# Kernel optimization log

Measured on AMD Instinct MI355X. Metric: run time of the kernel, lower is better.

The kernel has to match this reference:

```python
import jax, jax.numpy as jnp
import numpy as np


def setup_inputs() -> dict:
    key = jax.random.key(0)
    ks = jax.random.split(key, 9)
    bs, d, K, h = 2048, 128, 256, 256
    s = 0.02  # weight init scale
    return {
        "xhat": jax.random.normal(ks[0], (bs, d), jnp.float32),
        "x": jax.random.normal(ks[1], (bs, d), jnp.float32),
        "codebook": jax.random.normal(ks[2], (K, d), jnp.float32),
        "Wc": jax.random.normal(ks[3], (d, 2 * d), jnp.float32) * s,
        "bc": jnp.zeros((d,), jnp.float32),
        "W1_0": jax.random.normal(ks[4], (h, d), jnp.float32) * s,
        "W2_0": jax.random.normal(ks[5], (d, h), jnp.float32) * s,
        "W1_1": jax.random.normal(ks[6], (h, d), jnp.float32) * s,
        "W2_1": jax.random.normal(ks[7], (d, h), jnp.float32) * s,
    }


def reference(xhat, x, codebook, Wc, bc, W1_0, W2_0, W1_1, W2_1):
    # QINCoStep.encode: evaluate all K codebook candidates per batch element.
    d = xhat.shape[1]
    # MLPconcat on concat([zqs, xhat], -1): split Wc [d, 2d] into codebook and xhat parts,
    # so we never materialize the (bs*K, 2d) concatenated tensor.
    Wz, Wx = Wc[:, :d], Wc[:, d:]
    z = (codebook + codebook @ Wz.T)[None, :, :] + (xhat @ Wx.T)[:, None, :] + bc  # [bs, K, d]
    for W1, W2 in ((W1_0, W2_0), (W1_1, W2_1)):
        z = z + jax.nn.relu(jnp.einsum("bkd,hd->bkh", z, W1)) @ W2.T
    cand = z + xhat[:, None, :]  # [bs, K, d] candidate reconstructions
    dist = jnp.sum(jnp.square(cand - x[:, None, :]), axis=-1)  # [bs, K]
    codes = jnp.argmin(dist, axis=1)  # [bs]
    xhat_next = jnp.take_along_axis(cand, codes[:, None, None], axis=1)[:, 0]  # [bs, d]
    return codes, xhat_next - xhat
```

## Files before the change

kernel.cpp:

```cpp
#include <hip/hip_runtime.h>


typedef short bf8_t __attribute__((ext_vector_type(8)));
typedef float f32x16 __attribute__((ext_vector_type(16)));

__device__ inline unsigned short f2bh(float x) {
    unsigned u = __float_as_uint(x);
    u += 0x7fffu + ((u >> 16) & 1u);
    return (unsigned short)(u >> 16);
}
__device__ inline f32x16 mfma_bf(uint4 a, uint4 b, f32x16 c) {
    bf8_t av = __builtin_bit_cast(bf8_t, a);
    bf8_t bv = __builtin_bit_cast(bf8_t, b);
    return __builtin_amdgcn_mfma_f32_32x32x16_bf16(av, bv, c, 0, 0, 0);
}
__device__ inline unsigned packhi(float x, float y) {
    return __builtin_amdgcn_perm(__float_as_uint(y), __float_as_uint(x), 0x07060302u);
}

#define DELTA 6.0f

__global__ __launch_bounds__(256) void k_prep1(
    const float* __restrict__ Wc,
    const float* __restrict__ W1a, const float* __restrict__ W2a,
    const float* __restrict__ W1b, const float* __restrict__ W2b,
    float* __restrict__ WzT, float* __restrict__ WxT,
    float* __restrict__ W1Ta, float* __restrict__ W2Ta,
    float* __restrict__ W1Tb, float* __restrict__ W2Tb,
    uint4* __restrict__ F)
{
    int g = blockIdx.x * 256 + threadIdx.x;
    if (g < 16384) {
        int j = g >> 7, d = g & 127;
        WzT[g] = Wc[d * 256 + j];
    } else if (g < 32768) {
        int e = g - 16384; int j = e >> 7, d = e & 127;
        WxT[e] = Wc[d * 256 + 128 + j];
    } else if (g < 65536) {
        int e = g - 32768; int d = e >> 8, h = e & 255;
        W1Ta[e] = W1a[h * 128 + d];
    } else if (g < 98304) {
        int e = g - 65536; int h = e >> 7, i = e & 127;
        W2Ta[e] = W2a[i * 256 + h];
    } else if (g < 131072) {
        int e = g - 98304; int d = e >> 8, h = e & 255;
        W1Tb[e] = W1b[h * 128 + d];
    } else if (g < 163840) {
        int e = g - 131072; int h = e >> 7, i = e & 127;
        W2Tb[e] = W2b[i * 256 + h];
    } else if (g < 176128) {
        int idx = g - 163840;
        int mat = idx >> 12, fp = idx & 4095;
        int tile = fp >> 6, lane = fp & 63;
        const float* src;
        if (mat == 1) {
            int mt = tile >> 3, kt = tile & 7;
            src = W1b + (32 * mt + (lane & 31)) * 128 + 16 * kt + 8 * (lane >> 5);
        } else {
            const float* W = (mat == 0) ? W2a : W2b;
            int mt = tile >> 4, kt = tile & 15;
            src = W + (32 * mt + (lane & 31)) * 256 + 16 * kt + 8 * (lane >> 5);
        }
        unsigned short hs[8];
#pragma unroll
        for (int j = 0; j < 8; ++j) hs[j] = f2bh(src[j]);
        uint4 hv;
        hv.x = (unsigned)hs[0] | ((unsigned)hs[1] << 16);
        hv.y = (unsigned)hs[2] | ((unsigned)hs[3] << 16);
        hv.z = (unsigned)hs[4] | ((unsigned)hs[5] << 16);
        hv.w = (unsigned)hs[6] | ((unsigned)hs[7] << 16);
        F[idx] = hv;
    }
}

__global__ __launch_bounds__(256) void k_prep_k(
    const float* __restrict__ cb, const float* __restrict__ bc,
    const float* __restrict__ WzT, const float* __restrict__ W1T0,
    float* __restrict__ z0, float* __restrict__ H1f32)
{
    __shared__ float clds[4][128];
    __shared__ float zlds[4][128];
    const int t = threadIdx.x;
    const int r0 = blockIdx.x * 4;
#pragma unroll
    for (int e = t; e < 512; e += 256)
        clds[e >> 7][e & 127] = cb[(r0 + (e >> 7)) * 128 + (e & 127)];
    __syncthreads();
    {
        const int d = t & 127, r = t >> 7;
        float a0 = bc[d] + clds[r][d], a1 = bc[d] + clds[r + 2][d];
        for (int j = 0; j < 128; ++j) {
            const float w = WzT[j * 128 + d];
            a0 = fmaf(clds[r][j], w, a0);
            a1 = fmaf(clds[r + 2][j], w, a1);
        }
        z0[(r0 + r) * 128 + d] = a0;
        z0[(r0 + r + 2) * 128 + d] = a1;
        zlds[r][d] = a0; zlds[r + 2][d] = a1;
    }
    __syncthreads();
    {
        float a[4] = {0.f, 0.f, 0.f, 0.f};
        for (int d = 0; d < 128; ++d) {
            const float w = W1T0[d * 256 + t];
#pragma unroll
            for (int r = 0; r < 4; ++r) a[r] = fmaf(zlds[r][d], w, a[r]);
        }
        const int kt = t >> 4, half = (t >> 3) & 1, j = t & 7;
#pragma unroll
        for (int r = 0; r < 4; ++r) {
            int k = r0 + r; int kg = k >> 5, col = k & 31;
            H1f32[(((kg * 16 + kt) * 64) + half * 32 + col) * 8 + j] = a[r];
        }
    }
}

__global__ __launch_bounds__(256) void k_prep_b(
    const float* __restrict__ xhat, const float* __restrict__ WxT,
    const float* __restrict__ W1T0,
    float* __restrict__ u, float* __restrict__ U1)
{
    __shared__ float xlds[4][128];
    __shared__ float ulds[4][128];
    const int t = threadIdx.x;
    const int r0 = blockIdx.x * 4;
#pragma unroll
    for (int e = t; e < 512; e += 256)
        xlds[e >> 7][e & 127] = xhat[(r0 + (e >> 7)) * 128 + (e & 127)];
    __syncthreads();
    {
        const int d = t & 127, r = t >> 7;
        float a0 = 0.f, a1 = 0.f;
        for (int j = 0; j < 128; ++j) {
            const float w = WxT[j * 128 + d];
            a0 = fmaf(xlds[r][j], w, a0);
            a1 = fmaf(xlds[r + 2][j], w, a1);
        }
        u[(r0 + r) * 128 + d] = a0;
        u[(r0 + r + 2) * 128 + d] = a1;
        ulds[r][d] = a0; ulds[r + 2][d] = a1;
    }
    __syncthreads();
    {
        float a[4] = {0.f, 0.f, 0.f, 0.f};
        for (int d = 0; d < 128; ++d) {
            const float w = W1T0[d * 256 + t];
#pragma unroll
            for (int r = 0; r < 4; ++r) a[r] = fmaf(ulds[r][d], w, a[r]);
        }
#pragma unroll
        for (int r = 0; r < 4; ++r)
            U1[(r0 + r) * 256 + t] = a[r];
    }
}

__global__ __launch_bounds__(512, 6) void k_dist_approx(
    const float* __restrict__ z0, const float* __restrict__ u,
    const float* __restrict__ xhat, const float* __restrict__ x,
    const float* __restrict__ H1f32, const float* __restrict__ U1,
    const uint4* __restrict__ W2f0, const uint4* __restrict__ W1f1,
    const uint4* __restrict__ W2f1,
    int2* __restrict__ pairs, int* __restrict__ npairs)
{
    __shared__ uint4 Zf[2048];
    __shared__ uint4 Hf[1024];

    const int t = threadIdx.x;
    const int lane = t & 63, wave = t >> 6;
    const int wm = wave & 3, wn = wave >> 2;
    const int l31 = lane & 31, l5 = lane >> 5;
    const int b = blockIdx.x >> 1, q = blockIdx.x & 1;
    const int k0 = q << 7;

    f32x16 zs[2];
    {
        const float* ur = u + b * 128;
#pragma unroll
        for (int g = 0; g < 2; ++g) {
            const int col = ((wn << 1) + g) * 32 + l31;
            const float* zr = z0 + (k0 + col) * 128;
#pragma unroll
            for (int rg = 0; rg < 4; ++rg) {
                const int d0 = 32 * wm + 8 * rg + 4 * l5;
                float4 a = *(const float4*)(zr + d0);
                float4 c = *(const float4*)(ur + d0);
                zs[g][4*rg+0] = a.x + c.x;
                zs[g][4*rg+1] = a.y + c.y;
                zs[g][4*rg+2] = a.z + c.z;
                zs[g][4*rg+3] = a.w + c.w;
            }
        }
    }

#pragma unroll 1
    for (int r = 0; r < 4; ++r) {
        {
            const int kt = 4 * r + wm;
            const float4* up = (const float4*)(U1 + b * 256 + kt * 16 + 8 * l5);
            float4 ua = up[0], ub = up[1];
#pragma unroll
            for (int gi = 0; gi < 2; ++gi) {
                const int cg = (wn << 1) + gi;
                const int kg = (q << 2) + cg;
                const float4* hp = (const float4*)(H1f32 + (((kg * 16 + kt) * 64) + lane) * 8);
                float4 ha = hp[0], hb = hp[1];
                float v0 = fmaxf(ha.x + ua.x, 0.f), v1 = fmaxf(ha.y + ua.y, 0.f);
                float v2 = fmaxf(ha.z + ua.z, 0.f), v3 = fmaxf(ha.w + ua.w, 0.f);
                float v4 = fmaxf(hb.x + ub.x, 0.f), v5 = fmaxf(hb.y + ub.y, 0.f);
                float v6 = fmaxf(hb.z + ub.z, 0.f), v7 = fmaxf(hb.w + ub.w, 0.f);
                uint4 o;
                o.x = packhi(v0, v1); o.y = packhi(v2, v3);
                o.z = packhi(v4, v5); o.w = packhi(v6, v7);
                Hf[((cg << 2) + wm) * 64 + lane] = o;
            }
        }
        __syncthreads();
#pragma unroll
        for (int ktl = 0; ktl < 4; ++ktl) {
            uint4 ah = W2f0[((wm << 4) + 4 * r + ktl) * 64 + lane];
#pragma unroll
            for (int g = 0; g < 2; ++g) {
                uint4 bv = Hf[((((wn << 1) + g) << 2) + ktl) * 64 + lane];
                zs[g] = mfma_bf(ah, bv, zs[g]);
            }
        }
        __syncthreads();
    }

#pragma unroll
    for (int g = 0; g < 2; ++g) {
        const int cg = (wn << 1) + g;
#pragma unroll
        for (int rg = 0; rg < 4; ++rg) {
            uint2 hv;
            hv.x = packhi(zs[g][4*rg+0], zs[g][4*rg+1]);
            hv.y = packhi(zs[g][4*rg+2], zs[g][4*rg+3]);
            uint2* zb2 = (uint2*)&Zf[((cg << 3) + 2 * wm + (rg >> 1)) * 64];
            zb2[(((rg & 1) << 5) + l31) * 2 + l5] = hv;
        }
    }
    __syncthreads();

    const int tile = wave & 1, cg1 = wave >> 1;
#pragma unroll 1
    for (int c = 0; c < 4; ++c) {
        f32x16 acc;
#pragma unroll
        for (int rr = 0; rr < 16; ++rr) acc[rr] = 0.f;
        {
            const uint4* pw1 = W1f1 + ((2 * c + tile) << 3) * 64;
#pragma unroll
            for (int kt = 0; kt < 8; ++kt) {
                uint4 bv = Zf[((cg1 << 3) + kt) * 64 + lane];
                uint4 ah = pw1[kt * 64 + lane];
                acc = mfma_bf(ah, bv, acc);
            }
        }
        __syncthreads();
#pragma unroll
        for (int rg = 0; rg < 4; ++rg) {
            float v0 = fmaxf(acc[4*rg+0], 0.f), v1 = fmaxf(acc[4*rg+1], 0.f);
            float v2 = fmaxf(acc[4*rg+2], 0.f), v3 = fmaxf(acc[4*rg+3], 0.f);
            uint2 hv; hv.x = packhi(v0, v1); hv.y = packhi(v2, v3);
            uint2* hb2 = (uint2*)&Hf[((cg1 << 2) + (tile << 1) + (rg >> 1)) * 64];
            hb2[(((rg & 1) << 5) + l31) * 2 + l5] = hv;
        }
        __syncthreads();
#pragma unroll
        for (int ktl = 0; ktl < 4; ++ktl) {
            uint4 ah = W2f1[((wm << 4) + 4 * c + ktl) * 64 + lane];
#pragma unroll
            for (int g = 0; g < 2; ++g) {
                uint4 bv = Hf[((((wn << 1) + g) << 2) + ktl) * 64 + lane];
                zs[g] = mfma_bf(ah, bv, zs[g]);
            }
        }
    }

    float* red   = (float*)Hf;
    float* sdist = (float*)Hf + 512;
    int*   sk    = (int*)((float*)Hf + 640);
    __syncthreads();
#pragma unroll
    for (int g = 0; g < 2; ++g) {
        float s = 0.f;
        const int col = ((wn << 1) + g) * 32 + l31;
#pragma unroll
        for (int rg = 0; rg < 4; ++rg) {
            const int d0 = 32 * wm + 8 * rg + 4 * l5;
            float4 xh = *(const float4*)(xhat + b * 128 + d0);
            float4 xx = *(const float4*)(x + b * 128 + d0);
            float v;
            v = zs[g][4*rg+0] + xh.x - xx.x; s = fmaf(v, v, s);
            v = zs[g][4*rg+1] + xh.y - xx.y; s = fmaf(v, v, s);
            v = zs[g][4*rg+2] + xh.z - xx.z; s = fmaf(v, v, s);
            v = zs[g][4*rg+3] + xh.w - xx.w; s = fmaf(v, v, s);
        }
        s += __shfl_xor(s, 32, 64);
        if (l5 == 0) red[wm * 128 + col] = s;
    }
    __syncthreads();
    if (t < 128)
        sdist[t] = red[t] + red[128 + t] + red[256 + t] + red[384 + t];
    __syncthreads();
    int base = 0;
    if (wave == 0) {
        float v0 = sdist[lane], v1 = sdist[lane + 64];
        float m = fminf(v0, v1);
#pragma unroll
        for (int off = 32; off > 0; off >>= 1) m = fminf(m, __shfl_xor(m, off, 64));
        const float thr = m + DELTA;
        const unsigned long long below = (1ull << lane) - 1;
        float vv[2] = {v0, v1};
#pragma unroll
        for (int j = 0; j < 2; ++j) {
            bool p = vv[j] <= thr;
            unsigned long long mask = __ballot(p);
            int pos = base + __popcll(mask & below);
            if (p && pos < 8) sk[pos] = k0 + 64 * j + lane;
            base += __popcll(mask);
        }
    }
    __syncthreads();
    if (t == 0) {
        int c = base > 8 ? 8 : base;
        int off = atomicAdd(npairs, c);
        for (int s = 0; s < c; ++s)
            pairs[off + s] = make_int2(b, sk[s]);
    }
}

__global__ __launch_bounds__(256) void k_exact(
    const float* __restrict__ z0, const float* __restrict__ u,
    const float* __restrict__ xhat, const float* __restrict__ x,
    const int2* __restrict__ pairs, const int* __restrict__ npairs,
    const float* __restrict__ W1Ta, const float* __restrict__ W2Ta,
    const float* __restrict__ W1Tb, const float* __restrict__ W2Tb,
    unsigned long long* __restrict__ packed)
{
    __shared__ float z8[8][128];
    __shared__ float h8[8][256];
    __shared__ int pb[8], pk[8];
    __shared__ int scnt;
    __shared__ float part[8][32];
    const int t = threadIdx.x;
    if (t == 0) {
        int np = *npairs; if (np > 32768) np = 32768;
        int c = np - (int)blockIdx.x * 8;
        scnt = c < 0 ? 0 : (c > 8 ? 8 : c);
    }
    __syncthreads();
    const int cnt = scnt;
    if (cnt == 0) return;
    if (t < 8) {
        int idx = blockIdx.x * 8 + (t < cnt ? t : cnt - 1);
        int2 p = pairs[idx];
        pb[t] = p.x; pk[t] = p.y;
    }
    __syncthreads();
#pragma unroll
    for (int n = 0; n < 4; ++n) {
        int e = n * 256 + t; int r = e >> 7, d = e & 127;
        z8[r][d] = z0[pk[r] * 128 + d] + u[pb[r] * 128 + d];
    }
    __syncthreads();
    const float* W1T = W1Ta; const float* W2T = W2Ta;
#pragma unroll 1
    for (int blk = 0; blk < 2; ++blk) {
        float a1[8] = {0.f,0.f,0.f,0.f,0.f,0.f,0.f,0.f};
        for (int d = 0; d < 128; ++d) {
            const float w = W1T[d * 256 + t];
#pragma unroll
            for (int r = 0; r < 8; ++r) a1[r] = fmaf(z8[r][d], w, a1[r]);
        }
#pragma unroll
        for (int r = 0; r < 8; ++r) h8[r][t] = fmaxf(a1[r], 0.f);
        __syncthreads();
        const int ig = t & 127, rg = (t >> 7) * 4;
        float a2[4] = {0.f,0.f,0.f,0.f};
        for (int h = 0; h < 256; ++h) {
            const float w = W2T[h * 128 + ig];
#pragma unroll
            for (int j = 0; j < 4; ++j) a2[j] = fmaf(h8[rg + j][h], w, a2[j]);
        }
        __syncthreads();
#pragma unroll
        for (int j = 0; j < 4; ++j) z8[rg + j][ig] += a2[j];
        __syncthreads();
        W1T = W1Tb; W2T = W2Tb;
    }
    {
        const int r = t >> 5, c = t & 31;
        const int br = pb[r];
        float s = 0.f;
#pragma unroll
        for (int i = 0; i < 4; ++i) {
            int d = c * 4 + i;
            float v = z8[r][d] + xhat[br * 128 + d] - x[br * 128 + d];
            s = fmaf(v, v, s);
        }
        part[r][c] = s;
    }
    __syncthreads();
    if (t < 8 && t < cnt) {
        float s = 0.f;
#pragma unroll
        for (int c2 = 0; c2 < 32; ++c2) s += part[t][c2];
        unsigned long long pk64 = (((unsigned long long)__float_as_uint(s)) << 32)
                                | (unsigned long long)(unsigned)pk[t];
        atomicMin(&packed[pb[t]], pk64);
    }
}

__global__ __launch_bounds__(256) void k_final(
    const float* __restrict__ z0, const float* __restrict__ u,
    const unsigned long long* __restrict__ packed,
    const float* __restrict__ W1Ta, const float* __restrict__ W2Ta,
    const float* __restrict__ W1Tb, const float* __restrict__ W2Tb,
    float* __restrict__ out0, float* __restrict__ outd)
{
    __shared__ float z8[8][128];
    __shared__ float h8[8][256];
    __shared__ int ci[8];
    const int t = threadIdx.x;
    const int b0 = blockIdx.x * 8;
    if (t < 8) {
        int code = (int)(packed[b0 + t] & 0xFFFFFFFFull);
        ci[t] = code;
        out0[b0 + t] = (float)code;
    }
    __syncthreads();
#pragma unroll
    for (int n = 0; n < 4; ++n) {
        int e = n * 256 + t; int r = e >> 7, d = e & 127;
        z8[r][d] = z0[ci[r] * 128 + d] + u[(b0 + r) * 128 + d];
    }
    __syncthreads();
    const float* W1T = W1Ta; const float* W2T = W2Ta;
#pragma unroll 1
    for (int blk = 0; blk < 2; ++blk) {
        float a1[8] = {0.f,0.f,0.f,0.f,0.f,0.f,0.f,0.f};
        for (int d = 0; d < 128; ++d) {
            const float w = W1T[d * 256 + t];
#pragma unroll
            for (int r = 0; r < 8; ++r) a1[r] = fmaf(z8[r][d], w, a1[r]);
        }
#pragma unroll
        for (int r = 0; r < 8; ++r) h8[r][t] = fmaxf(a1[r], 0.f);
        __syncthreads();
        const int ig = t & 127, rg = (t >> 7) * 4;
        float a2[4] = {0.f,0.f,0.f,0.f};
        for (int h = 0; h < 256; ++h) {
            const float w = W2T[h * 128 + ig];
#pragma unroll
            for (int j = 0; j < 4; ++j) a2[j] = fmaf(h8[rg + j][h], w, a2[j]);
        }
        __syncthreads();
#pragma unroll
        for (int j = 0; j < 4; ++j) z8[rg + j][ig] += a2[j];
        __syncthreads();
        W1T = W1Tb; W2T = W2Tb;
    }
#pragma unroll
    for (int n = 0; n < 4; ++n) {
        int e = n * 256 + t; int r = e >> 7, d = e & 127;
        outd[(b0 + r) * 128 + d] = z8[r][d];
    }
}

extern "C" void kernel_launch(void* const* d_in, const int* in_sizes, int n_in,
                              void* d_out, int out_size, void* d_ws, size_t ws_size,
                              hipStream_t stream) {
    const float* xhat = (const float*)d_in[0];
    const float* x    = (const float*)d_in[1];
    const float* cb   = (const float*)d_in[2];
    const float* Wc   = (const float*)d_in[3];
    const float* bc   = (const float*)d_in[4];
    const float* W1_0 = (const float*)d_in[5];
    const float* W2_0 = (const float*)d_in[6];
    const float* W1_1 = (const float*)d_in[7];
    const float* W2_1 = (const float*)d_in[8];
    float* out = (float*)d_out;
    float* ws  = (float*)d_ws;

    float* WzT   = ws + 0;
    float* WxT   = ws + 16384;
    float* W1T0  = ws + 32768;
    float* W2T0  = ws + 65536;
    float* W1T1  = ws + 98304;
    float* W2T1  = ws + 131072;
    float* z0    = ws + 163840;
    float* u     = ws + 196608;
    float* H1f32 = ws + 458752;
    float* U1    = ws + 524288;
    uint4* F     = (uint4*)(ws + 1048576);
    const uint4* W2f0 = F;
    const uint4* W1f1 = F + 4096;
    const uint4* W2f1 = F + 8192;
    int2*  pairs  = (int2*)(ws + 1097728);
    int*   npairs = (int*)(ws + 1163264);
    unsigned long long* packed = (unsigned long long*)(ws + 1163268);

    k_prep1<<<688, 256, 0, stream>>>(Wc, W1_0, W2_0, W1_1, W2_1,
                                     WzT, WxT, W1T0, W2T0, W1T1, W2T1, F);
    k_prep_k<<<64, 256, 0, stream>>>(cb, bc, WzT, W1T0, z0, H1f32);
    k_prep_b<<<512, 256, 0, stream>>>(xhat, WxT, W1T0, u, U1);
    hipMemsetAsync(npairs, 0, 4, stream);
    hipMemsetAsync(packed, 0xFF, 2048 * 8, stream);
    k_dist_approx<<<4096, 512, 0, stream>>>(z0, u, xhat, x, H1f32, U1,
                                            W2f0, W1f1, W2f1, pairs, npairs);
    k_exact<<<4096, 256, 0, stream>>>(z0, u, xhat, x, pairs, npairs,
                                      W1T0, W2T0, W1T1, W2T1, packed);
    k_final<<<256, 256, 0, stream>>>(z0, u, packed,
                                     W1T0, W2T0, W1T1, W2T1, out, out + 2048);
}
```

Baseline: 322.3 us.

## Fuse prep kernels, store bf16 intermediates, merge exact rescoring with final output

Merges the codebook and batch precompute kernels into one launch and stores z0, u, H1 and U1 as bf16 so the approximate-distance kernel reads half the bytes. The atomic pair list, two memsets and the separate exact and final kernels are replaced by per-(batch, half) candidate slots. A single per-batch kernel rescores up to 16 candidates in fp32, picks the argmin and writes the output without 64-bit atomicMin. The DELTA filter margin is widened to offset the extra bf16 rounding, which can admit more candidates and risks borderline argmin decisions.

```diff
diff --git a/kernel.cpp b/kernel.cpp
--- a/kernel.cpp
+++ b/kernel.cpp
@@ -9,6 +9,9 @@
     u += 0x7fffu + ((u >> 16) & 1u);
     return (unsigned short)(u >> 16);
 }
+__device__ inline float bh2f(unsigned short h) {
+    return __uint_as_float(((unsigned)h) << 16);
+}
 __device__ inline f32x16 mfma_bf(uint4 a, uint4 b, f32x16 c) {
     bf8_t av = __builtin_bit_cast(bf8_t, a);
     bf8_t bv = __builtin_bit_cast(bf8_t, b);
@@ -17,8 +20,13 @@
 __device__ inline unsigned packhi(float x, float y) {
     return __builtin_amdgcn_perm(__float_as_uint(y), __float_as_uint(x), 0x07060302u);
 }
-
-#define DELTA 6.0f
+__device__ inline unsigned addrelu2t(unsigned hv, unsigned uv) {
+    float a0 = __uint_as_float(hv << 16) + __uint_as_float(uv << 16);
+    float a1 = __uint_as_float(hv & 0xFFFF0000u) + __uint_as_float(uv & 0xFFFF0000u);
+    return packhi(fmaxf(a0, 0.f), fmaxf(a1, 0.f));
+}
+
+#define DELTA 6.5f
 
 __global__ __launch_bounds__(256) void k_prep1(
     const float* __restrict__ Wc,
@@ -73,30 +81,41 @@
     }
 }
 
-__global__ __launch_bounds__(256) void k_prep_k(
+__global__ __launch_bounds__(256) void k_prep2(
     const float* __restrict__ cb, const float* __restrict__ bc,
-    const float* __restrict__ WzT, const float* __restrict__ W1T0,
-    float* __restrict__ z0, float* __restrict__ H1f32)
+    const float* __restrict__ xhat,
+    const float* __restrict__ WzT, const float* __restrict__ WxT,
+    const float* __restrict__ W1T0,
+    float* __restrict__ z0, unsigned short* __restrict__ z0bf,
+    unsigned short* __restrict__ H1bf,
+    float* __restrict__ u, unsigned short* __restrict__ ubf,
+    unsigned short* __restrict__ U1bf)
 {
-    __shared__ float clds[4][128];
-    __shared__ float zlds[4][128];
+    __shared__ float src[4][128];
+    __shared__ float res[4][128];
     const int t = threadIdx.x;
-    const int r0 = blockIdx.x * 4;
+    const bool krole = blockIdx.x < 64;
+    const int r0 = (krole ? blockIdx.x : (blockIdx.x - 64)) * 4;
+    const float* in = krole ? cb : xhat;
+    const float* WT = krole ? WzT : WxT;
 #pragma unroll
     for (int e = t; e < 512; e += 256)
-        clds[e >> 7][e & 127] = cb[(r0 + (e >> 7)) * 128 + (e & 127)];
+        src[e >> 7][e & 127] = in[(r0 + (e >> 7)) * 128 + (e & 127)];
     __syncthreads();
     {
         const int d = t & 127, r = t >> 7;
-        float a0 = bc[d] + clds[r][d], a1 = bc[d] + clds[r + 2][d];
+        float a0 = krole ? (bc[d] + src[r][d]) : 0.f;
+        float a1 = krole ? (bc[d] + src[r + 2][d]) : 0.f;
         for (int j = 0; j < 128; ++j) {
-            const float w = WzT[j * 128 + d];
-            a0 = fmaf(clds[r][j], w, a0);
-            a1 = fmaf(clds[r + 2][j], w, a1);
-        }
-        z0[(r0 + r) * 128 + d] = a0;
-        z0[(r0 + r + 2) * 128 + d] = a1;
-        zlds[r][d] = a0; zlds[r + 2][d] = a1;
+            const float w = WT[j * 128 + d];
+            a0 = fmaf(src[r][j], w, a0);
+            a1 = fmaf(src[r + 2][j], w, a1);
+        }
+        float* dst = krole ? z0 : u;
+        unsigned short* dstbf = krole ? z0bf : ubf;
+        dst[(r0 + r) * 128 + d] = a0;        dstbf[(r0 + r) * 128 + d] = f2bh(a0);
+        dst[(r0 + r + 2) * 128 + d] = a1;    dstbf[(r0 + r + 2) * 128 + d] = f2bh(a1);
+        res[r][d] = a0; res[r + 2][d] = a1;
     }
     __syncthreads();
     {
@@ -104,63 +123,30 @@
         for (int d = 0; d < 128; ++d) {
             const float w = W1T0[d * 256 + t];
 #pragma unroll
-            for (int r = 0; r < 4; ++r) a[r] = fmaf(zlds[r][d], w, a[r]);
-        }
-        const int kt = t >> 4, half = (t >> 3) & 1, j = t & 7;
-#pragma unroll
-        for (int r = 0; r < 4; ++r) {
-            int k = r0 + r; int kg = k >> 5, col = k & 31;
-            H1f32[(((kg * 16 + kt) * 64) + half * 32 + col) * 8 + j] = a[r];
-        }
-    }
-}
-
-__global__ __launch_bounds__(256) void k_prep_b(
-    const float* __restrict__ xhat, const float* __restrict__ WxT,
-    const float* __restrict__ W1T0,
-    float* __restrict__ u, float* __restrict__ U1)
-{
-    __shared__ float xlds[4][128];
-    __shared__ float ulds[4][128];
-    const int t = threadIdx.x;
-    const int r0 = blockIdx.x * 4;
-#pragma unroll
-    for (int e = t; e < 512; e += 256)
-        xlds[e >> 7][e & 127] = xhat[(r0 + (e >> 7)) * 128 + (e & 127)];
-    __syncthreads();
-    {
-        const int d = t & 127, r = t >> 7;
-        float a0 = 0.f, a1 = 0.f;
-        for (int j = 0; j < 128; ++j) {
-            const float w = WxT[j * 128 + d];
-            a0 = fmaf(xlds[r][j], w, a0);
-            a1 = fmaf(xlds[r + 2][j], w, a1);
-        }
-        u[(r0 + r) * 128 + d] = a0;
-        u[(r0 + r + 2) * 128 + d] = a1;
-        ulds[r][d] = a0; ulds[r + 2][d] = a1;
-    }
-    __syncthreads();
-    {
-        float a[4] = {0.f, 0.f, 0.f, 0.f};
-        for (int d = 0; d < 128; ++d) {
-            const float w = W1T0[d * 256 + t];
-#pragma unroll
-            for (int r = 0; r < 4; ++r) a[r] = fmaf(ulds[r][d], w, a[r]);
-        }
-#pragma unroll
-        for (int r = 0; r < 4; ++r)
-            U1[(r0 + r) * 256 + t] = a[r];
+            for (int r = 0; r < 4; ++r) a[r] = fmaf(res[r][d], w, a[r]);
+        }
+        if (krole) {
+            const int kt = t >> 4, half = (t >> 3) & 1, j = t & 7;
+#pragma unroll
+            for (int r = 0; r < 4; ++r) {
+                int k = r0 + r; int kg = k >> 5, col = k & 31;
+                H1bf[(((kg * 16 + kt) * 64) + half * 32 + col) * 8 + j] = f2bh(a[r]);
+            }
+        } else {
+#pragma unroll
+            for (int r = 0; r < 4; ++r)
+                U1bf[(r0 + r) * 256 + t] = f2bh(a[r]);
+        }
     }
 }
 
 __global__ __launch_bounds__(512, 6) void k_dist_approx(
-    const float* __restrict__ z0, const float* __restrict__ u,
+    const unsigned short* __restrict__ z0bf, const unsigned short* __restrict__ ubf,
     const float* __restrict__ xhat, const float* __restrict__ x,
-    const float* __restrict__ H1f32, const float* __restrict__ U1,
+    const uint4* __restrict__ H1u4, const unsigned short* __restrict__ U1bf,
     const uint4* __restrict__ W2f0, const uint4* __restrict__ W1f1,
     const uint4* __restrict__ W2f1,
-    int2* __restrict__ pairs, int* __restrict__ npairs)
+    int* __restrict__ cand, int* __restrict__ cnt)
 {
     __shared__ uint4 Zf[2048];
     __shared__ uint4 Hf[1024];
@@ -174,20 +160,20 @@
 
     f32x16 zs[2];
     {
-        const float* ur = u + b * 128;
+        const unsigned short* ur = ubf + b * 128;
 #pragma unroll
         for (int g = 0; g < 2; ++g) {
             const int col = ((wn << 1) + g) * 32 + l31;
-            const float* zr = z0 + (k0 + col) * 128;
+            const unsigned short* zr = z0bf + (k0 + col) * 128;
 #pragma unroll
             for (int rg = 0; rg < 4; ++rg) {
                 const int d0 = 32 * wm + 8 * rg + 4 * l5;
-                float4 a = *(const float4*)(zr + d0);
-                float4 c = *(const float4*)(ur + d0);
-                zs[g][4*rg+0] = a.x + c.x;
-                zs[g][4*rg+1] = a.y + c.y;
-                zs[g][4*rg+2] = a.z + c.z;
-                zs[g][4*rg+3] = a.w + c.w;
+                ushort4 a = *(const ushort4*)(zr + d0);
+                ushort4 c = *(const ushort4*)(ur + d0);
+                zs[g][4*rg+0] = bh2f(a.x) + bh2f(c.x);
+                zs[g][4*rg+1] = bh2f(a.y) + bh2f(c.y);
+                zs[g][4*rg+2] = bh2f(a.z) + bh2f(c.z);
+                zs[g][4*rg+3] = bh2f(a.w) + bh2f(c.w);
             }
         }
     }
@@ -196,21 +182,17 @@
     for (int r = 0; r < 4; ++r) {
         {
             const int kt = 4 * r + wm;
-            const float4* up = (const float4*)(U1 + b * 256 + kt * 16 + 8 * l5);
-            float4 ua = up[0], ub = up[1];
+            const uint4 uv = *(const uint4*)(U1bf + b * 256 + kt * 16 + 8 * l5);
 #pragma unroll
             for (int gi = 0; gi < 2; ++gi) {
                 const int cg = (wn << 1) + gi;
                 const int kg = (q << 2) + cg;
-                const float4* hp = (const float4*)(H1f32 + (((kg * 16 + kt) * 64) + lane) * 8);
-                float4 ha = hp[0], hb = hp[1];
-                float v0 = fmaxf(ha.x + ua.x, 0.f), v1 = fmaxf(ha.y + ua.y, 0.f);
-                float v2 = fmaxf(ha.z + ua.z, 0.f), v3 = fmaxf(ha.w + ua.w, 0.f);
-                float v4 = fmaxf(hb.x + ub.x, 0.f), v5 = fmaxf(hb.y + ub.y, 0.f);
-                float v6 = fmaxf(hb.z + ub.z, 0.f), v7 = fmaxf(hb.w + ub.w, 0.f);
+                uint4 hv = H1u4[(kg * 16 + kt) * 64 + lane];
                 uint4 o;
-                o.x = packhi(v0, v1); o.y = packhi(v2, v3);
-                o.z = packhi(v4, v5); o.w = packhi(v6, v7);
+                o.x = addrelu2t(hv.x, uv.x);
+                o.y = addrelu2t(hv.y, uv.y);
+                o.z = addrelu2t(hv.z, uv.z);
+                o.w = addrelu2t(hv.w, uv.w);
                 Hf[((cg << 2) + wm) * 64 + lane] = o;
             }
         }
@@ -303,8 +285,8 @@
     if (t < 128)
         sdist[t] = red[t] + red[128 + t] + red[256 + t] + red[384 + t];
     __syncthreads();
-    int base = 0;
     if (wave == 0) {
+        int base = 0;
         float v0 = sdist[lane], v1 = sdist[lane + 64];
         float m = fminf(v0, v1);
 #pragma unroll
@@ -320,152 +302,105 @@
             if (p && pos < 8) sk[pos] = k0 + 64 * j + lane;
             base += __popcll(mask);
         }
-    }
-    __syncthreads();
-    if (t == 0) {
-        int c = base > 8 ? 8 : base;
-        int off = atomicAdd(npairs, c);
-        for (int s = 0; s < c; ++s)
-            pairs[off + s] = make_int2(b, sk[s]);
-    }
-}
-
-__global__ __launch_bounds__(256) void k_exact(
+        if (lane == 0) {
+            int c = base > 8 ? 8 : base;
+            cnt[b * 2 + q] = c;
+            for (int s2 = 0; s2 < c; ++s2)
+                cand[(b * 2 + q) * 8 + s2] = sk[s2];
+        }
+    }
+}
+
+__global__ __launch_bounds__(256) void k_final2(
     const float* __restrict__ z0, const float* __restrict__ u,
     const float* __restrict__ xhat, const float* __restrict__ x,
-    const int2* __restrict__ pairs, const int* __restrict__ npairs,
-    const float* __restrict__ W1Ta, const float* __restrict__ W2Ta,
-    const float* __restrict__ W1Tb, const float* __restrict__ W2Tb,
-    unsigned long long* __restrict__ packed)
-{
-    __shared__ float z8[8][128];
-    __shared__ float h8[8][256];
-    __shared__ int pb[8], pk[8];
-    __shared__ int scnt;
-    __shared__ float part[8][32];
-    const int t = threadIdx.x;
-    if (t == 0) {
-        int np = *npairs; if (np > 32768) np = 32768;
-        int c = np - (int)blockIdx.x * 8;
-        scnt = c < 0 ? 0 : (c > 8 ? 8 : c);
-    }
-    __syncthreads();
-    const int cnt = scnt;
-    if (cnt == 0) return;
-    if (t < 8) {
-        int idx = blockIdx.x * 8 + (t < cnt ? t : cnt - 1);
-        int2 p = pairs[idx];
-        pb[t] = p.x; pk[t] = p.y;
-    }
-    __syncthreads();
-#pragma unroll
-    for (int n = 0; n < 4; ++n) {
-        int e = n * 256 + t; int r = e >> 7, d = e & 127;
-        z8[r][d] = z0[pk[r] * 128 + d] + u[pb[r] * 128 + d];
-    }
-    __syncthreads();
-    const float* W1T = W1Ta; const float* W2T = W2Ta;
-#pragma unroll 1
-    for (int blk = 0; blk < 2; ++blk) {
-        float a1[8] = {0.f,0.f,0.f,0.f,0.f,0.f,0.f,0.f};
-        for (int d = 0; d < 128; ++d) {
-            const float w = W1T[d * 256 + t];
-#pragma unroll
-            for (int r = 0; r < 8; ++r) a1[r] = fmaf(z8[r][d], w, a1[r]);
-        }
-#pragma unroll
-        for (int r = 0; r < 8; ++r) h8[r][t] = fmaxf(a1[r], 0.f);
-        __syncthreads();
-        const int ig = t & 127, rg = (t >> 7) * 4;
-        float a2[4] = {0.f,0.f,0.f,0.f};
-        for (int h = 0; h < 256; ++h) {
-            const float w = W2T[h * 128 + ig];
-#pragma unroll
-            for (int j = 0; j < 4; ++j) a2[j] = fmaf(h8[rg + j][h], w, a2[j]);
-        }
-        __syncthreads();
-#pragma unroll
-        for (int j = 0; j < 4; ++j) z8[rg + j][ig] += a2[j];
-        __syncthreads();
-        W1T = W1Tb; W2T = W2Tb;
-    }
-    {
-        const int r = t >> 5, c = t & 31;
-        const int br = pb[r];
-        float s = 0.f;
-#pragma unroll
-        for (int i = 0; i < 4; ++i) {
-            int d = c * 4 + i;
-            float v = z8[r][d] + xhat[br * 128 + d] - x[br * 128 + d];
-            s = fmaf(v, v, s);
-        }
-        part[r][c] = s;
-    }
-    __syncthreads();
-    if (t < 8 && t < cnt) {
-        float s = 0.f;
-#pragma unroll
-        for (int c2 = 0; c2 < 32; ++c2) s += part[t][c2];
-        unsigned long long pk64 = (((unsigned long long)__float_as_uint(s)) << 32)
-                                | (unsigned long long)(unsigned)pk[t];
-        atomicMin(&packed[pb[t]], pk64);
-    }
-}
-
-__global__ __launch_bounds__(256) void k_final(
-    const float* __restrict__ z0, const float* __restrict__ u,
-    const unsigned long long* __restrict__ packed,
+    const int* __restrict__ cand, const int* __restrict__ cnt,
     const float* __restrict__ W1Ta, const float* __restrict__ W2Ta,
     const float* __restrict__ W1Tb, const float* __restrict__ W2Tb,
     float* __restrict__ out0, float* __restrict__ outd)
 {
-    __shared__ float z8[8][128];
+    __shared__ float z16[16][128];
     __shared__ float h8[8][256];
-    __shared__ int ci[8];
-    const int t = threadIdx.x;
-    const int b0 = blockIdx.x * 8;
-    if (t < 8) {
-        int code = (int)(packed[b0 + t] & 0xFFFFFFFFull);
-        ci[t] = code;
-        out0[b0 + t] = (float)code;
-    }
-    __syncthreads();
-#pragma unroll
-    for (int n = 0; n < 4; ++n) {
-        int e = n * 256 + t; int r = e >> 7, d = e & 127;
-        z8[r][d] = z0[ci[r] * 128 + d] + u[(b0 + r) * 128 + d];
-    }
-    __syncthreads();
-    const float* W1T = W1Ta; const float* W2T = W2Ta;
+    __shared__ int ck[16];
+    __shared__ float dd[16];
+    __shared__ int widx;
+    const int t = threadIdx.x, b = blockIdx.x;
+    const int c0 = cnt[2 * b], c1 = cnt[2 * b + 1];
+    const int tot = c0 + c1;
+    if (t < 16) {
+        int k;
+        if (t < c0)          k = cand[2 * b * 8 + t];
+        else if (t < tot)    k = cand[(2 * b + 1) * 8 + (t - c0)];
+        else                 k = cand[2 * b * 8];
+        ck[t] = k;
+    }
+    __syncthreads();
+    const int nb = (tot > 8) ? 2 : 1;
 #pragma unroll 1
-    for (int blk = 0; blk < 2; ++blk) {
-        float a1[8] = {0.f,0.f,0.f,0.f,0.f,0.f,0.f,0.f};
-        for (int d = 0; d < 128; ++d) {
-            const float w = W1T[d * 256 + t];
-#pragma unroll
-            for (int r = 0; r < 8; ++r) a1[r] = fmaf(z8[r][d], w, a1[r]);
-        }
-#pragma unroll
-        for (int r = 0; r < 8; ++r) h8[r][t] = fmaxf(a1[r], 0.f);
+    for (int batch = 0; batch < nb; ++batch) {
+        const int bo = batch * 8;
+        const float* ub = u + b * 128;
+#pragma unroll
+        for (int n = 0; n < 4; ++n) {
+            int e = n * 256 + t; int r = e >> 7, d = e & 127;
+            z16[bo + r][d] = z0[ck[bo + r] * 128 + d] + ub[d];
+        }
         __syncthreads();
-        const int ig = t & 127, rg = (t >> 7) * 4;
-        float a2[4] = {0.f,0.f,0.f,0.f};
-        for (int h = 0; h < 256; ++h) {
-            const float w = W2T[h * 128 + ig];
-#pragma unroll
-            for (int j = 0; j < 4; ++j) a2[j] = fmaf(h8[rg + j][h], w, a2[j]);
-        }
-        __syncthreads();
-#pragma unroll
-        for (int j = 0; j < 4; ++j) z8[rg + j][ig] += a2[j];
-        __syncthreads();
-        W1T = W1Tb; W2T = W2Tb;
-    }
-#pragma unroll
-    for (int n = 0; n < 4; ++n) {
-        int e = n * 256 + t; int r = e >> 7, d = e & 127;
-        outd[(b0 + r) * 128 + d] = z8[r][d];
-    }
+        const float* W1T = W1Ta; const float* W2T = W2Ta;
+#pragma unroll 1
+        for (int blk = 0; blk < 2; ++blk) {
+            float a1[8] = {0.f,0.f,0.f,0.f,0.f,0.f,0.f,0.f};
+            for (int d = 0; d < 128; ++d) {
+                const float w = W1T[d * 256 + t];
+#pragma unroll
+                for (int r = 0; r < 8; ++r) a1[r] = fmaf(z16[bo + r][d], w, a1[r]);
+            }
+#pragma unroll
+            for (int r = 0; r < 8; ++r) h8[r][t] = fmaxf(a1[r], 0.f);
+            __syncthreads();
+            const int ig = t & 127, rg = (t >> 7) * 4;
+            float a2[4] = {0.f,0.f,0.f,0.f};
+            for (int h = 0; h < 256; ++h) {
+                const float w = W2T[h * 128 + ig];
+#pragma unroll
+                for (int j = 0; j < 4; ++j) a2[j] = fmaf(h8[rg + j][h], w, a2[j]);
+            }
+            __syncthreads();
+#pragma unroll
+            for (int j = 0; j < 4; ++j) z16[bo + rg + j][ig] += a2[j];
+            __syncthreads();
+            W1T = W1Tb; W2T = W2Tb;
+        }
+        {
+            float* part = (float*)h8;
+            const int r = t >> 5, c = t & 31;
+            float s = 0.f;
+#pragma unroll
+            for (int i = 0; i < 4; ++i) {
+                int d = c * 4 + i;
+                float v = z16[bo + r][d] + xhat[b * 128 + d] - x[b * 128 + d];
+                s = fmaf(v, v, s);
+            }
+            part[r * 32 + c] = s;
+            __syncthreads();
+            if (t < 8) {
+                float ssum = 0.f;
+#pragma unroll
+                for (int c2 = 0; c2 < 32; ++c2) ssum += part[t * 32 + c2];
+                dd[bo + t] = ssum;
+            }
+            __syncthreads();
+        }
+    }
+    if (t == 0) {
+        float bv = dd[0]; int w = 0;
+        for (int s = 1; s < tot; ++s)
+            if (dd[s] < bv) { bv = dd[s]; w = s; }
+        widx = w;
+        out0[b] = (float)ck[w];
+    }
+    __syncthreads();
+    if (t < 128) outd[b * 128 + t] = z16[widx][t];
 }
 
 extern "C" void kernel_launch(void* const* d_in, const int* in_sizes, int n_in,
@@ -491,26 +426,23 @@
     float* W2T1  = ws + 131072;
     float* z0    = ws + 163840;
     float* u     = ws + 196608;
-    float* H1f32 = ws + 458752;
-    float* U1    = ws + 524288;
-    uint4* F     = (uint4*)(ws + 1048576);
+    unsigned short* z0bf = (unsigned short*)(ws + 458752);
+    unsigned short* ubf  = (unsigned short*)(ws + 475136);
+    unsigned short* U1bf = (unsigned short*)(ws + 606208);
+    unsigned short* H1bf = (unsigned short*)(ws + 868352);
+    uint4* F     = (uint4*)(ws + 901120);
     const uint4* W2f0 = F;
     const uint4* W1f1 = F + 4096;
     const uint4* W2f1 = F + 8192;
-    int2*  pairs  = (int2*)(ws + 1097728);
-    int*   npairs = (int*)(ws + 1163264);
-    unsigned long long* packed = (unsigned long long*)(ws + 1163268);
+    int* cand = (int*)(ws + 950272);
+    int* cnt  = (int*)(ws + 983040);
 
     k_prep1<<<688, 256, 0, stream>>>(Wc, W1_0, W2_0, W1_1, W2_1,
                                      WzT, WxT, W1T0, W2T0, W1T1, W2T1, F);
-    k_prep_k<<<64, 256, 0, stream>>>(cb, bc, WzT, W1T0, z0, H1f32);
-    k_prep_b<<<512, 256, 0, stream>>>(xhat, WxT, W1T0, u, U1);
-    hipMemsetAsync(npairs, 0, 4, stream);
-    hipMemsetAsync(packed, 0xFF, 2048 * 8, stream);
-    k_dist_approx<<<4096, 512, 0, stream>>>(z0, u, xhat, x, H1f32, U1,
-                                            W2f0, W1f1, W2f1, pairs, npairs);
-    k_exact<<<4096, 256, 0, stream>>>(z0, u, xhat, x, pairs, npairs,
-                                      W1T0, W2T0, W1T1, W2T1, packed);
-    k_final<<<256, 256, 0, stream>>>(z0, u, packed,
-                                     W1T0, W2T0, W1T1, W2T1, out, out + 2048);
-}
+    k_prep2<<<576, 256, 0, stream>>>(cb, bc, xhat, WzT, WxT, W1T0,
+                                     z0, z0bf, H1bf, u, ubf, U1bf);
+    k_dist_approx<<<4096, 512, 0, stream>>>(z0bf, ubf, xhat, x, (const uint4*)H1bf,
+                                            U1bf, W2f0, W1f1, W2f1, cand, cnt);
+    k_final2<<<2048, 256, 0, stream>>>(z0, u, xhat, x, cand, cnt,
+                                       W1T0, W2T0, W1T1, W2T1, out, out + 2048);
+}
```

Measured after the change: 339.9 us. 1.05x slower.
